# Kernel tuning notes

Measured on AMD Instinct MI355X. Metric: run time of the kernel, lower is better.

## Reference

```python
import math
import jax, jax.numpy as jnp
import numpy as np

N_HEAD = 16

def setup_inputs() -> dict:
    key = jax.random.key(0)
    k1, k2, k3 = jax.random.split(key, 3)
    B, T, C = 4, 2048, 1024
    x = jax.random.normal(k1, (B, T, C), dtype=jnp.float32)
    Wqkv = jax.random.normal(k2, (C, 3 * C), dtype=jnp.float32) * (1.0 / math.sqrt(C))
    bqkv = jnp.zeros((3 * C,), dtype=jnp.float32)
    Wproj = jax.random.normal(k3, (C, C), dtype=jnp.float32) * (1.0 / math.sqrt(C))
    bproj = jnp.zeros((C,), dtype=jnp.float32)
    return {"x": x, "Wqkv": Wqkv, "bqkv": bqkv, "Wproj": Wproj, "bproj": bproj}

def reference(x, Wqkv, bqkv, Wproj, bproj):
    B, T, C = x.shape
    H = N_HEAD
    D = C // H
    # fused QKV projection
    qkv = x @ Wqkv + bqkv                      # [B,T,3C]
    qkv = qkv.reshape(B, T, 3, H, D).transpose(0, 2, 3, 1, 4)  # [B,3,H,T,D]
    q, k, v = qkv[:, 0], qkv[:, 1], qkv[:, 2]  # each [B,H,T,D]
    scale = 1.0 / math.sqrt(D)
    att = jnp.einsum('bhtd,bhsd->bhts', q, k) * scale  # [B,H,T,T]
    # causal mask: disallow s > t
    mask = jnp.triu(jnp.ones((T, T), dtype=bool), k=1)
    att = jnp.where(mask, jnp.float32(-1e9), att)
    att = jax.nn.softmax(att, axis=-1)
    y = jnp.einsum('bhts,bhsd->bhtd', att, v)  # [B,H,T,D]
    y = y.transpose(0, 2, 1, 3).reshape(B, T, C)
    y = y @ Wproj + bproj
    return y
```

## Files before the change

kernel.cpp:

```cpp
#include <hip/hip_runtime.h>
#include <hip/hip_bf16.h>

#define B_ 4
#define T_ 2048
#define C_ 1024
#define H_ 16
#define D_ 64

typedef __attribute__((ext_vector_type(8))) short short8;
typedef __attribute__((ext_vector_type(4))) float f32x4;

#define QSCALE 0.18033688011112042f

static __device__ __forceinline__ unsigned short f2bf(float f) {
  unsigned u = __float_as_uint(f);
  u += 0x7fff + ((u >> 16) & 1);
  return (unsigned short)(u >> 16);
}

static __device__ __forceinline__ unsigned cvt_pk_bf16(float lo, float hi) {
  unsigned r;
  asm("v_cvt_pk_bf16_f32 %0, %1, %2" : "=v"(r) : "v"(lo), "v"(hi));
  return r;
}

static __device__ __forceinline__ float fast_exp2(float x) {
#if __has_builtin(__builtin_amdgcn_exp2f)
  return __builtin_amdgcn_exp2f(x);
#else
  return exp2f(x);
#endif
}

#define GL2LDS16(g, l)                                              \
  __builtin_amdgcn_global_load_lds(                                 \
      (const __attribute__((address_space(1))) void*)(g),           \
      (__attribute__((address_space(3))) void*)(l), 16, 0, 0)

__global__ __launch_bounds__(256) void prepass(
    const float* __restrict__ x, const float* __restrict__ Wq,
    const float* __restrict__ Wp, ushort* __restrict__ xb,
    ushort* __restrict__ Wqt, ushort* __restrict__ Wpt) {
  __shared__ ushort tile[32][33];
  const int bid = blockIdx.x;
  if (bid < 8192) {
    const size_t i = ((size_t)bid * 256 + threadIdx.x) * 4;
    float4 vv = *(const float4*)(x + i);
    ushort4 o = {f2bf(vv.x), f2bf(vv.y), f2bf(vv.z), f2bf(vv.w)};
    *(ushort4*)(xb + i) = o;
    return;
  }
  const float* in;
  ushort* out;
  int N, tix;
  if (bid < 8192 + 3072) {
    in = Wq; out = Wqt; N = 3 * C_; tix = bid - 8192;
  } else {
    in = Wp; out = Wpt; N = C_; tix = bid - 11264;
  }
  const int nT = N >> 5;
  const int k0 = (tix / nT) << 5, n0 = (tix % nT) << 5;
  const int r = threadIdx.x >> 3;
  const int c4 = (threadIdx.x & 7) << 2;
  float4 v = *(const float4*)(in + (size_t)(k0 + r) * N + n0 + c4);
  tile[c4 + 0][r] = f2bf(v.x);
  tile[c4 + 1][r] = f2bf(v.y);
  tile[c4 + 2][r] = f2bf(v.z);
  tile[c4 + 3][r] = f2bf(v.w);
  __syncthreads();
  ushort4 o = {tile[r][c4], tile[r][c4 + 1], tile[r][c4 + 2], tile[r][c4 + 3]};
  *(ushort4*)(out + (size_t)(n0 + r) * C_ + k0 + c4) = o;
}

static __device__ __forceinline__ void swz_src64(int wave, int lane, int p,
                                                 int& row, int& offU) {
  const int flat = p * 4096 + wave * 1024 + lane * 16;
  row = flat >> 7;
  const int pos = (flat & 127) >> 4;
  const int x = pos ^ (row & 7);
  offU = x * 8;
}
static __device__ __forceinline__ int swz_frag64(int r, int quad, int ko) {
  return r * 128 + (((quad | (ko << 2)) ^ (r & 7)) << 4);
}

__global__ __launch_bounds__(512, 2) void gemm_qkv_mfma(
    const ushort* __restrict__ A, const ushort* __restrict__ Bt,
    const float* __restrict__ bias, ushort* __restrict__ q,
    ushort* __restrict__ k, ushort* __restrict__ v) {
  __shared__ __align__(16) ushort KA[3][128 * 64];
  __shared__ __align__(16) ushort KB[3][256 * 64];
  const int wave = threadIdx.x >> 6, lane = threadIdx.x & 63;
  const int c = lane & 15, quad = lane >> 4;
  const int wm = wave >> 2, wn = wave & 3;
  const int bid0 = blockIdx.x;
  const int bid = (bid0 & 7) * 96 + (bid0 >> 3);
  const int m0 = (bid / 12) << 7;
  const int n0 = (bid % 12) << 8;

  int aRow[2], aX[2], bRow[4], bX[4];
#pragma unroll
  for (int p = 0; p < 2; ++p) {
    const int flat = p * 8192 + (int)threadIdx.x * 16;
    aRow[p] = flat >> 7;
    aX[p] = (((flat & 127) >> 4) ^ (aRow[p] & 7)) * 8;
  }
#pragma unroll
  for (int p = 0; p < 4; ++p) {
    const int flat = p * 8192 + (int)threadIdx.x * 16;
    bRow[p] = flat >> 7;
    bX[p] = (((flat & 127) >> 4) ^ (bRow[p] & 7)) * 8;
  }
  int fOffA[2][4], fOffB[2][4];
#pragma unroll
  for (int ko = 0; ko < 2; ++ko) {
#pragma unroll
    for (int i = 0; i < 4; ++i)
      fOffA[ko][i] = swz_frag64(wm * 64 + i * 16 + c, quad, ko);
#pragma unroll
    for (int j = 0; j < 4; ++j)
      fOffB[ko][j] = swz_frag64(wn * 64 + j * 16 + c, quad, ko);
  }

  f32x4 acc[4][4];
#pragma unroll
  for (int i = 0; i < 4; ++i)
#pragma unroll
    for (int j = 0; j < 4; ++j) acc[i][j] = (f32x4){0.f, 0.f, 0.f, 0.f};

#pragma unroll
  for (int p = 0; p < 4; ++p)
    GL2LDS16(Bt + (size_t)(n0 + bRow[p]) * C_ + bX[p],
             (char*)KB[0] + p * 8192 + wave * 1024);
#pragma unroll
  for (int p = 0; p < 2; ++p)
    GL2LDS16(A + (size_t)(m0 + aRow[p]) * C_ + aX[p],
             (char*)KA[0] + p * 8192 + wave * 1024);
#pragma unroll
  for (int p = 0; p < 4; ++p)
    GL2LDS16(Bt + (size_t)(n0 + bRow[p]) * C_ + 64 + bX[p],
             (char*)KB[1] + p * 8192 + wave * 1024);
#pragma unroll
  for (int p = 0; p < 2; ++p)
    GL2LDS16(A + (size_t)(m0 + aRow[p]) * C_ + 64 + aX[p],
             (char*)KA[1] + p * 8192 + wave * 1024);
  asm volatile("s_waitcnt vmcnt(6)" ::: "memory");
  __builtin_amdgcn_s_barrier();

  int cur = 0, s2 = 2;
  for (int kt = 0; kt < 16; ++kt) {
    const int kk2 = (kt + 2) << 6;
    const bool more = (kt + 2) < 16;
    const char* la = (const char*)KA[cur];
    const char* lb = (const char*)KB[cur];
    short8 af[4][2], bf0[2][2], bf1[2][2];

#pragma unroll
    for (int i = 0; i < 4; ++i)
#pragma unroll
      for (int ko = 0; ko < 2; ++ko) af[i][ko] = *(const short8*)(la + fOffA[ko][i]);
#pragma unroll
    for (int d = 0; d < 2; ++d)
#pragma unroll
      for (int ko = 0; ko < 2; ++ko) bf0[d][ko] = *(const short8*)(lb + fOffB[ko][d]);
    if (more) {
      GL2LDS16(Bt + (size_t)(n0 + bRow[0]) * C_ + kk2 + bX[0],
               (char*)KB[s2] + 0 * 8192 + wave * 1024);
      GL2LDS16(Bt + (size_t)(n0 + bRow[1]) * C_ + kk2 + bX[1],
               (char*)KB[s2] + 1 * 8192 + wave * 1024);
      GL2LDS16(A + (size_t)(m0 + aRow[0]) * C_ + kk2 + aX[0],
               (char*)KA[s2] + 0 * 8192 + wave * 1024);
    }
    __builtin_amdgcn_s_barrier();
    __builtin_amdgcn_s_setprio(1);
#pragma unroll
    for (int i = 0; i < 4; ++i)
#pragma unroll
      for (int dj = 0; dj < 2; ++dj)
#pragma unroll
        for (int ko = 0; ko < 2; ++ko)
          acc[i][dj] = __builtin_amdgcn_mfma_f32_16x16x32_bf16(
              af[i][ko], bf0[dj][ko], acc[i][dj], 0, 0, 0);
    __builtin_amdgcn_s_setprio(0);
    __builtin_amdgcn_s_barrier();

#pragma unroll
    for (int d = 0; d < 2; ++d)
#pragma unroll
      for (int ko = 0; ko < 2; ++ko)
        bf1[d][ko] = *(const short8*)(lb + fOffB[ko][2 + d]);
    if (more) {
      GL2LDS16(Bt + (size_t)(n0 + bRow[2]) * C_ + kk2 + bX[2],
               (char*)KB[s2] + 2 * 8192 + wave * 1024);
      GL2LDS16(Bt + (size_t)(n0 + bRow[3]) * C_ + kk2 + bX[3],
               (char*)KB[s2] + 3 * 8192 + wave * 1024);
      GL2LDS16(A + (size_t)(m0 + aRow[1]) * C_ + kk2 + aX[1],
               (char*)KA[s2] + 1 * 8192 + wave * 1024);
    }
    __builtin_amdgcn_s_barrier();
    __builtin_amdgcn_s_setprio(1);
#pragma unroll
    for (int i = 0; i < 4; ++i)
#pragma unroll
      for (int dj = 0; dj < 2; ++dj)
#pragma unroll
        for (int ko = 0; ko < 2; ++ko)
          acc[i][2 + dj] = __builtin_amdgcn_mfma_f32_16x16x32_bf16(
              af[i][ko], bf1[dj][ko], acc[i][2 + dj], 0, 0, 0);
    __builtin_amdgcn_s_setprio(0);
    __builtin_amdgcn_s_barrier();

    if (kt + 1 < 16) {
      if (more)
        asm volatile("s_waitcnt vmcnt(6)" ::: "memory");
      else
        asm volatile("s_waitcnt vmcnt(0)" ::: "memory");
      __builtin_amdgcn_s_barrier();
    }
    cur = (cur == 2) ? 0 : cur + 1;
    s2 = (s2 == 2) ? 0 : s2 + 1;
  }

  const int s = n0 >> 10;
  if (s == 2) {
#pragma unroll
    for (int j = 0; j < 4; ++j) {
      const int n = n0 + wn * 64 + j * 16 + c;
      const int h = (n >> 6) & 15, d = n & 63;
      const float bval = bias[n];
#pragma unroll
      for (int i = 0; i < 4; ++i) {
        const int m = m0 + wm * 64 + i * 16 + quad * 4;
        const int b = m >> 11, t = m & 2047;
        ushort4 pk = {f2bf(acc[i][j][0] + bval), f2bf(acc[i][j][1] + bval),
                      f2bf(acc[i][j][2] + bval), f2bf(acc[i][j][3] + bval)};
        *(ushort4*)(v + (((size_t)((b << 4) + h) << 6) + d) * T_ + t) = pk;
      }
    }
  } else {
    ushort* outp = (s == 0) ? q : k;
    const float sc = (s == 0) ? QSCALE : 1.0f;
#pragma unroll
    for (int j = 0; j < 4; ++j) {
      const int n = n0 + wn * 64 + j * 16 + c;
      const int h = (n >> 6) & 15, d = n & 63;
      const float bval = bias[n];
#pragma unroll
      for (int i = 0; i < 4; ++i) {
#pragma unroll
        for (int r = 0; r < 4; ++r) {
          const int m = m0 + wm * 64 + i * 16 + quad * 4 + r;
          const int b = m >> 11, t = m & 2047;
          outp[(((size_t)((b << 4) + h) << 11) + t) * 64 + d] =
              f2bf((acc[i][j][r] + bval) * sc);
        }
      }
    }
  }
}

__global__ __launch_bounds__(256) void gemm_proj_mfma(
    const ushort* __restrict__ A, const ushort* __restrict__ Bt,
    const float* __restrict__ bias, float* __restrict__ out) {
  __shared__ __align__(16) ushort As[2][128 * 64];
  __shared__ __align__(16) ushort Bs[2][128 * 64];
  const int tid = threadIdx.x;
  const int wave = tid >> 6, lane = tid & 63;
  const int c = lane & 15, quad = lane >> 4;
  const int wm = wave & 1, wn = wave >> 1;
  const int bid0 = blockIdx.y * 8 + blockIdx.x;
  const int bid = (bid0 & 7) * 64 + (bid0 >> 3);
  const int m0 = (bid >> 3) << 7;
  const int n0 = (bid & 7) << 7;

  int sRow[4], sOff[4];
#pragma unroll
  for (int p = 0; p < 4; ++p) swz_src64(wave, lane, p, sRow[p], sOff[p]);
  int fOffA[2][4], fOffB[2][4];
#pragma unroll
  for (int ko = 0; ko < 2; ++ko) {
#pragma unroll
    for (int i = 0; i < 4; ++i)
      fOffA[ko][i] = swz_frag64(wm * 64 + i * 16 + c, quad, ko);
#pragma unroll
    for (int j = 0; j < 4; ++j)
      fOffB[ko][j] = swz_frag64(wn * 64 + j * 16 + c, quad, ko);
  }

  f32x4 acc[4][4];
#pragma unroll
  for (int i = 0; i < 4; ++i)
#pragma unroll
    for (int j = 0; j < 4; ++j) acc[i][j] = (f32x4){0.f, 0.f, 0.f, 0.f};

#define PROJ_STAGE(buf, kk)                                            \
  do {                                                                 \
    _Pragma("unroll") for (int p = 0; p < 4; ++p) {                    \
      GL2LDS16(A + (size_t)(m0 + sRow[p]) * C_ + (kk) + sOff[p],       \
               (char*)As[buf] + p * 4096 + wave * 1024);               \
      GL2LDS16(Bt + (size_t)(n0 + sRow[p]) * C_ + (kk) + sOff[p],      \
               (char*)Bs[buf] + p * 4096 + wave * 1024);               \
    }                                                                  \
  } while (0)

  PROJ_STAGE(0, 0);
  int cur = 0;
  for (int k0 = 0; k0 < C_; k0 += 64) {
    __syncthreads();
    if (k0 + 64 < C_) PROJ_STAGE(cur ^ 1, k0 + 64);
#pragma unroll
    for (int ko = 0; ko < 2; ++ko) {
      short8 af[4], bf[4];
#pragma unroll
      for (int i = 0; i < 4; ++i)
        af[i] = *(const short8*)((const char*)As[cur] + fOffA[ko][i]);
#pragma unroll
      for (int j = 0; j < 4; ++j)
        bf[j] = *(const short8*)((const char*)Bs[cur] + fOffB[ko][j]);
      __builtin_amdgcn_s_setprio(1);
#pragma unroll
      for (int i = 0; i < 4; ++i)
#pragma unroll
        for (int j = 0; j < 4; ++j)
          acc[i][j] = __builtin_amdgcn_mfma_f32_16x16x32_bf16(af[i], bf[j],
                                                              acc[i][j], 0, 0, 0);
      __builtin_amdgcn_s_setprio(0);
    }
    cur ^= 1;
  }
#undef PROJ_STAGE

#pragma unroll
  for (int j = 0; j < 4; ++j) {
    const int n = n0 + wn * 64 + j * 16 + c;
    const float bval = bias[n];
#pragma unroll
    for (int i = 0; i < 4; ++i) {
#pragma unroll
      for (int r = 0; r < 4; ++r) {
        const int m = m0 + wm * 64 + i * 16 + quad * 4 + r;
        out[(size_t)m * C_ + n] = acc[i][j][r] + bval;
      }
    }
  }
}

__global__ __launch_bounds__(256) void attn(const ushort* __restrict__ q,
                                            const ushort* __restrict__ k,
                                            const ushort* __restrict__ v,
                                            ushort* __restrict__ y2) {
  const int qt = 15 - (int)(blockIdx.x >> 6);
  const int bh = blockIdx.x & 63;
  const int t0 = qt << 7;
  const int w = threadIdx.x >> 6;
  const int lane = threadIdx.x & 63;
  const int c = lane & 15;
  const int quad = lane >> 4;

  const ushort* qp = q + (size_t)bh * T_ * D_;
  const ushort* kp = k + (size_t)bh * T_ * D_;
  const ushort* vp = v + (size_t)bh * D_ * T_;

  __shared__ __align__(16) ushort Ks[2][64 * 64];
  __shared__ __align__(16) ushort Vs[2][64 * 64];

  short8 qf[2][2];
#pragma unroll
  for (int g = 0; g < 2; ++g) {
    const ushort* qrow = qp + (size_t)(t0 + 32 * w + 16 * g + c) * D_;
    qf[g][0] = *(const short8*)(qrow + quad * 8);
    qf[g][1] = *(const short8*)(qrow + 32 + quad * 8);
  }

  int sRow[2], sX[2];
#pragma unroll
  for (int p = 0; p < 2; ++p) {
    const int flat = p * 4096 + (int)threadIdx.x * 16;
    sRow[p] = flat >> 7;
    sX[p] = (((flat & 127) >> 4) ^ (sRow[p] & 7)) * 8;
  }

#define STAGE(buf, s0s)                                                   \
  do {                                                                    \
    _Pragma("unroll") for (int p = 0; p < 2; ++p) {                       \
      GL2LDS16(kp + (size_t)((s0s) + sRow[p]) * D_ + sX[p],               \
               (char*)Ks[buf] + p * 4096 + w * 1024);                     \
      GL2LDS16(vp + (size_t)sRow[p] * T_ + (s0s) + sX[p],                 \
               (char*)Vs[buf] + p * 4096 + w * 1024);                     \
    }                                                                     \
  } while (0)

  f32x4 o[2][4];
  float l_i[2] = {0.f, 0.f};
#pragma unroll
  for (int g = 0; g < 2; ++g)
#pragma unroll
    for (int dt = 0; dt < 4; ++dt) o[g][dt] = (f32x4){0.f, 0.f, 0.f, 0.f};

  const int nb = 2 * qt + 2;
  STAGE(0, 0);
  int cur = 0;
  const int sA = c + ((quad & 1) << 5);
  const int sB = sA + 16;

  for (int ib = 0; ib < nb; ++ib) {
    const int s0 = ib << 6;
    __syncthreads();
    if (ib + 1 < nb) STAGE(cur ^ 1, s0 + 64);

    f32x4 st[2][4];
    __builtin_amdgcn_s_setprio(1);
#pragma unroll
    for (int kt = 0; kt < 4; ++kt) {
      const char* kb = (const char*)Ks[cur];
      short8 af0 = *(const short8*)(kb + swz_frag64(kt * 16 + c, quad, 0));
      short8 af1 = *(const short8*)(kb + swz_frag64(kt * 16 + c, quad, 1));
#pragma unroll
      for (int g = 0; g < 2; ++g) {
        f32x4 a = (f32x4){0.f, 0.f, 0.f, 0.f};
        a = __builtin_amdgcn_mfma_f32_16x16x32_bf16(af0, qf[g][0], a, 0, 0, 0);
        a = __builtin_amdgcn_mfma_f32_16x16x32_bf16(af1, qf[g][1], a, 0, 0, 0);
        st[g][kt] = a;
      }
    }
    __builtin_amdgcn_s_setprio(0);

    unsigned pw[2][4][2];
#pragma unroll
    for (int g = 0; g < 2; ++g) {
      const int qbase = t0 + 32 * w + 16 * g;
      if (s0 + 63 > qbase) {
#pragma unroll
        for (int kt = 0; kt < 4; ++kt)
#pragma unroll
          for (int r = 0; r < 4; ++r)
            if (s0 + kt * 16 + 4 * quad + r > qbase + c) st[g][kt][r] = -1e30f;
      }
      float lacc = 0.f;
#pragma unroll
      for (int kt = 0; kt < 4; ++kt) {
        float p0 = fast_exp2(st[g][kt][0]);
        float p1 = fast_exp2(st[g][kt][1]);
        float p2 = fast_exp2(st[g][kt][2]);
        float p3 = fast_exp2(st[g][kt][3]);
        lacc += (p0 + p1) + (p2 + p3);
        pw[g][kt][0] = cvt_pk_bf16(p0, p1);
        pw[g][kt][1] = cvt_pk_bf16(p2, p3);
      }
      l_i[g] += lacc;
    }

    short8 pf[2][2];
#pragma unroll
    for (int g = 0; g < 2; ++g) {
#pragma unroll
      for (int half = 0; half < 2; ++half) {
        const unsigned lo0 = pw[g][half * 2][0], lo1 = pw[g][half * 2][1];
        const unsigned hi0 = pw[g][half * 2 + 1][0], hi1 = pw[g][half * 2 + 1][1];
        const unsigned a0 = (unsigned)__shfl((int)lo0, sA);
        const unsigned b0 = (unsigned)__shfl((int)hi0, sA);
        const unsigned a1 = (unsigned)__shfl((int)lo1, sA);
        const unsigned b1 = (unsigned)__shfl((int)hi1, sA);
        const unsigned a2 = (unsigned)__shfl((int)lo0, sB);
        const unsigned b2 = (unsigned)__shfl((int)hi0, sB);
        const unsigned a3 = (unsigned)__shfl((int)lo1, sB);
        const unsigned b3 = (unsigned)__shfl((int)hi1, sB);
        uint4 r;
        r.x = (quad & 2) ? b0 : a0;
        r.y = (quad & 2) ? b1 : a1;
        r.z = (quad & 2) ? b2 : a2;
        r.w = (quad & 2) ? b3 : a3;
        pf[g][half] = *(short8*)&r;
      }
    }

    __builtin_amdgcn_s_setprio(1);
#pragma unroll
    for (int dt = 0; dt < 4; ++dt) {
      const char* vb = (const char*)Vs[cur];
      short8 vf0 = *(const short8*)(vb + swz_frag64(dt * 16 + c, quad, 0));
      short8 vf1 = *(const short8*)(vb + swz_frag64(dt * 16 + c, quad, 1));
#pragma unroll
      for (int g = 0; g < 2; ++g) {
        o[g][dt] =
            __builtin_amdgcn_mfma_f32_16x16x32_bf16(vf0, pf[g][0], o[g][dt], 0, 0, 0);
        o[g][dt] =
            __builtin_amdgcn_mfma_f32_16x16x32_bf16(vf1, pf[g][1], o[g][dt], 0, 0, 0);
      }
    }
    __builtin_amdgcn_s_setprio(0);
    cur ^= 1;
  }
#undef STAGE

  float linv[2];
#pragma unroll
  for (int g = 0; g < 2; ++g) {
    float ls = l_i[g];
    ls += __shfl_xor(ls, 16);
    ls += __shfl_xor(ls, 32);
    linv[g] = 1.0f / ls;
  }

  const int b = bh >> 4, h = bh & 15;
#pragma unroll
  for (int g = 0; g < 2; ++g) {
    const int row = t0 + 32 * w + 16 * g + c;
    ushort* dst = y2 + (size_t)(b * T_ + row) * C_ + h * 64;
#pragma unroll
    for (int dt = 0; dt < 4; ++dt) {
      uint2 ov = {cvt_pk_bf16(o[g][dt][0] * linv[g], o[g][dt][1] * linv[g]),
                  cvt_pk_bf16(o[g][dt][2] * linv[g], o[g][dt][3] * linv[g])};
      *(uint2*)(dst + dt * 16 + 4 * quad) = ov;
    }
  }
}

extern "C" void kernel_launch(void* const* d_in, const int* in_sizes, int n_in,
                              void* d_out, int out_size, void* d_ws,
                              size_t ws_size, hipStream_t stream) {
  const float* x = (const float*)d_in[0];
  const float* Wqkv = (const float*)d_in[1];
  const float* bqkv = (const float*)d_in[2];
  const float* Wproj = (const float*)d_in[3];
  const float* bproj = (const float*)d_in[4];
  float* out = (float*)d_out;

  const size_t per = (size_t)B_ * H_ * T_ * D_;
  ushort* q = (ushort*)d_ws;
  ushort* k = q + per;
  ushort* v = k + per;
  ushort* y2 = v + per;
  ushort* xb = y2 + per;
  ushort* Wqkvt = xb + per;
  ushort* Wprojt = Wqkvt + 3 * C_ * C_;

  prepass<<<dim3(12288), 256, 0, stream>>>(x, Wqkv, Wproj, xb, Wqkvt, Wprojt);
  gemm_qkv_mfma<<<dim3(768), 512, 0, stream>>>(xb, Wqkvt, bqkv, q, k, v);
  attn<<<dim3(1024), 256, 0, stream>>>(q, k, v, y2);
  gemm_proj_mfma<<<dim3(8, 64), 256, 0, stream>>>(y2, Wprojt, bproj, out);
}
```

Measured before the change: 249.3 us.

## Software-pipeline LDS fragment loads and cut barriers per QKV GEMM k-step

Restructures the QKV GEMM main loop so the A fragments and the first half of the B fragments for the next k-tile are loaded from LDS during the current tile's second MFMA batch, with the first fragments preloaded before the loop. Per-iteration barriers drop from four or five to one, paired with a combined vmcnt/lgkmcnt wait. The aim is to hide LDS read latency and barrier stalls behind MFMA work. The cost is more live registers for the double-buffered fragments and tighter correctness reliance on a single barrier guarding the triple-buffered LDS stages.

```diff
diff --git a/kernel.cpp b/kernel.cpp
--- a/kernel.cpp
+++ b/kernel.cpp
@@ -147,22 +147,35 @@
   asm volatile("s_waitcnt vmcnt(6)" ::: "memory");
   __builtin_amdgcn_s_barrier();
 
-  int cur = 0, s2 = 2;
+  short8 af[4][2], bfA[2][2], bfB[2][2];
+  {
+    const char* la0 = (const char*)KA[0];
+    const char* lb0 = (const char*)KB[0];
+#pragma unroll
+    for (int i = 0; i < 4; ++i)
+#pragma unroll
+      for (int ko = 0; ko < 2; ++ko)
+        af[i][ko] = *(const short8*)(la0 + fOffA[ko][i]);
+#pragma unroll
+    for (int d = 0; d < 2; ++d)
+#pragma unroll
+      for (int ko = 0; ko < 2; ++ko)
+        bfA[d][ko] = *(const short8*)(lb0 + fOffB[ko][d]);
+  }
+
+  int cur = 0;
   for (int kt = 0; kt < 16; ++kt) {
+    const int nxt = (cur == 2) ? 0 : cur + 1;
+    const int s2 = (nxt == 2) ? 0 : nxt + 1;
+    const char* lb = (const char*)KB[cur];
     const int kk2 = (kt + 2) << 6;
     const bool more = (kt + 2) < 16;
-    const char* la = (const char*)KA[cur];
-    const char* lb = (const char*)KB[cur];
-    short8 af[4][2], bf0[2][2], bf1[2][2];
-
-#pragma unroll
-    for (int i = 0; i < 4; ++i)
-#pragma unroll
-      for (int ko = 0; ko < 2; ++ko) af[i][ko] = *(const short8*)(la + fOffA[ko][i]);
+
 #pragma unroll
     for (int d = 0; d < 2; ++d)
 #pragma unroll
-      for (int ko = 0; ko < 2; ++ko) bf0[d][ko] = *(const short8*)(lb + fOffB[ko][d]);
+      for (int ko = 0; ko < 2; ++ko)
+        bfB[d][ko] = *(const short8*)(lb + fOffB[ko][2 + d]);
     if (more) {
       GL2LDS16(Bt + (size_t)(n0 + bRow[0]) * C_ + kk2 + bX[0],
                (char*)KB[s2] + 0 * 8192 + wave * 1024);
@@ -171,7 +184,6 @@
       GL2LDS16(A + (size_t)(m0 + aRow[0]) * C_ + kk2 + aX[0],
                (char*)KA[s2] + 0 * 8192 + wave * 1024);
     }
-    __builtin_amdgcn_s_barrier();
     __builtin_amdgcn_s_setprio(1);
 #pragma unroll
     for (int i = 0; i < 4; ++i)
@@ -180,15 +192,30 @@
 #pragma unroll
         for (int ko = 0; ko < 2; ++ko)
           acc[i][dj] = __builtin_amdgcn_mfma_f32_16x16x32_bf16(
-              af[i][ko], bf0[dj][ko], acc[i][dj], 0, 0, 0);
+              af[i][ko], bfA[dj][ko], acc[i][dj], 0, 0, 0);
     __builtin_amdgcn_s_setprio(0);
+
+    if (more)
+      asm volatile("s_waitcnt vmcnt(3) lgkmcnt(0)" ::: "memory");
+    else
+      asm volatile("s_waitcnt vmcnt(0) lgkmcnt(0)" ::: "memory");
     __builtin_amdgcn_s_barrier();
 
-#pragma unroll
-    for (int d = 0; d < 2; ++d)
-#pragma unroll
-      for (int ko = 0; ko < 2; ++ko)
-        bf1[d][ko] = *(const short8*)(lb + fOffB[ko][2 + d]);
+    short8 afN[4][2], bfAN[2][2];
+    if (kt + 1 < 16) {
+      const char* lan = (const char*)KA[nxt];
+      const char* lbn = (const char*)KB[nxt];
+#pragma unroll
+      for (int i = 0; i < 4; ++i)
+#pragma unroll
+        for (int ko = 0; ko < 2; ++ko)
+          afN[i][ko] = *(const short8*)(lan + fOffA[ko][i]);
+#pragma unroll
+      for (int d = 0; d < 2; ++d)
+#pragma unroll
+        for (int ko = 0; ko < 2; ++ko)
+          bfAN[d][ko] = *(const short8*)(lbn + fOffB[ko][d]);
+    }
     if (more) {
       GL2LDS16(Bt + (size_t)(n0 + bRow[2]) * C_ + kk2 + bX[2],
                (char*)KB[s2] + 2 * 8192 + wave * 1024);
@@ -197,7 +224,6 @@
       GL2LDS16(A + (size_t)(m0 + aRow[1]) * C_ + kk2 + aX[1],
                (char*)KA[s2] + 1 * 8192 + wave * 1024);
     }
-    __builtin_amdgcn_s_barrier();
     __builtin_amdgcn_s_setprio(1);
 #pragma unroll
     for (int i = 0; i < 4; ++i)
@@ -206,19 +232,19 @@
 #pragma unroll
         for (int ko = 0; ko < 2; ++ko)
           acc[i][2 + dj] = __builtin_amdgcn_mfma_f32_16x16x32_bf16(
-              af[i][ko], bf1[dj][ko], acc[i][2 + dj], 0, 0, 0);
+              af[i][ko], bfB[dj][ko], acc[i][2 + dj], 0, 0, 0);
     __builtin_amdgcn_s_setprio(0);
-    __builtin_amdgcn_s_barrier();
-
     if (kt + 1 < 16) {
-      if (more)
-        asm volatile("s_waitcnt vmcnt(6)" ::: "memory");
-      else
-        asm volatile("s_waitcnt vmcnt(0)" ::: "memory");
-      __builtin_amdgcn_s_barrier();
-    }
-    cur = (cur == 2) ? 0 : cur + 1;
-    s2 = (s2 == 2) ? 0 : s2 + 1;
+#pragma unroll
+      for (int i = 0; i < 4; ++i)
+#pragma unroll
+        for (int ko = 0; ko < 2; ++ko) af[i][ko] = afN[i][ko];
+#pragma unroll
+      for (int d = 0; d < 2; ++d)
+#pragma unroll
+        for (int ko = 0; ko < 2; ++ko) bfA[d][ko] = bfAN[d][ko];
+    }
+    cur = nxt;
   }
 
   const int s = n0 >> 10;
```

Measured after the change: 245.7 us. No clear change (-1.4%).
